# Kernel tuning notes

Measured on AMD Instinct MI355X. Metric: run time of the kernel, lower is better.

Reference implementation:

```python
import jax, jax.numpy as jnp
import numpy as np
from jax import lax

B, S, T = 128, 512, 256


def setup_inputs() -> dict:
    key = jax.random.key(0)
    k1, k2, k3, k4, k5, k6 = jax.random.split(key, 6)
    logits = jax.random.normal(k1, (B, S, T), dtype=jnp.float32)
    lengths = jax.random.randint(k2, (B,), S // 2, S + 1)
    mask = jnp.arange(S)[None, :] < lengths[:, None]  # [B,S] bool, mask[:,0] always True
    labels = jax.random.randint(k3, (B, S), 0, T)
    start_transitions = 0.1 * jax.random.normal(k4, (T,), dtype=jnp.float32)
    end_transitions = 0.1 * jax.random.normal(k5, (T,), dtype=jnp.float32)
    transitions = 0.1 * jax.random.normal(k6, (T, T), dtype=jnp.float32)
    return {"logits": logits, "mask": mask, "labels": labels,
            "start_transitions": start_transitions,
            "end_transitions": end_transitions,
            "transitions": transitions}


def _numerator(logits, tags, mask, start_t, end_t, trans):
    # Score of the gold tag path (torchcrf _compute_score), fully vectorized.
    b = jnp.arange(logits.shape[0])
    maskf = mask.astype(logits.dtype)
    emit = jnp.take_along_axis(logits, tags[..., None], axis=2)[..., 0]  # [B,S]
    score = start_t[tags[:, 0]] + emit[:, 0]
    tr = trans[tags[:, :-1], tags[:, 1:]]  # [B,S-1]
    score = score + jnp.sum((tr + emit[:, 1:]) * maskf[:, 1:], axis=1)
    lengths = mask.sum(axis=1)
    last_tags = tags[b, lengths - 1]
    return score + end_t[last_tags]


def _denominator(logits, mask, start_t, end_t, trans):
    # Forward algorithm (log partition), lax.scan over time.
    score0 = start_t[None, :] + logits[:, 0]  # [B,T]

    def step(score, xs):
        emit, m = xs  # emit [B,T], m [B]
        nxt = jax.nn.logsumexp(score[:, :, None] + trans[None, :, :]
                               + emit[:, None, :], axis=1)  # [B,T]
        return jnp.where(m[:, None], nxt, score), None

    emits = jnp.swapaxes(logits[:, 1:], 0, 1)  # [S-1,B,T]
    masks = mask[:, 1:].T  # [S-1,B]
    score, _ = lax.scan(step, score0, (emits, masks))
    return jax.nn.logsumexp(score + end_t[None, :], axis=1)  # [B]


def _viterbi(logits, mask, start_t, end_t, trans):
    # Viterbi decode with masking; masked steps carry score and use identity
    # backpointers so backtracing passes through padding correctly.
    Bn, Sn, Tn = logits.shape
    score0 = start_t[None, :] + logits[:, 0]  # [B,T]
    ident = jnp.arange(Tn, dtype=jnp.int32)[None, :]

    def step(score, xs):
        emit, m = xs
        cand = score[:, :, None] + trans[None, :, :]  # [B,T_prev,T_next]
        idx = jnp.argmax(cand, axis=1).astype(jnp.int32)  # [B,T]
        nxt = jnp.max(cand, axis=1) + emit
        score = jnp.where(m[:, None], nxt, score)
        hist = jnp.where(m[:, None], idx, ident)
        return score, hist

    emits = jnp.swapaxes(logits[:, 1:], 0, 1)
    masks = mask[:, 1:].T
    score, history = lax.scan(step, score0, (emits, masks))  # history [S-1,B,T]
    last = jnp.argmax(score + end_t[None, :], axis=1).astype(jnp.int32)  # [B]

    def back(tag, h):
        prev = jnp.take_along_axis(h, tag[:, None], axis=1)[:, 0]
        return prev, prev

    _, tags_prefix = lax.scan(back, last, history, reverse=True)  # [S-1,B]
    tags = jnp.concatenate([tags_prefix.T, last[:, None]], axis=1)  # [B,S]
    return jnp.where(mask, tags, 0)


def reference(logits, mask, labels, start_transitions, end_transitions, transitions):
    pred = _viterbi(logits, mask, start_transitions, end_transitions, transitions)
    num = _numerator(logits, labels, mask, start_transitions, end_transitions, transitions)
    den = _denominator(logits, mask, start_transitions, end_transitions, transitions)
    loss = -jnp.mean(num - den)  # torchcrf reduction='mean', negated
    return pred, loss
```

## Files before the change

kernel.cpp:

```cpp
#include <hip/hip_runtime.h>
#include <hip/hip_bf16.h>
#include <math.h>

#define Bn 128
#define Sn 512
#define Tn 256

typedef float vf64 __attribute__((ext_vector_type(64)));


__global__ void prep_kernel(const float* __restrict__ trans, float* __restrict__ transT) {
    int k = blockIdx.x * blockDim.x + threadIdx.x;
    transT[(k & 255) * 256 + (k >> 8)] = trans[k];
}

__launch_bounds__(512, 2)
__global__ void crf_fwd2_kernel(const float* __restrict__ logits,
                                const float* __restrict__ start_t,
                                const float* __restrict__ end_t,
                                const float* __restrict__ trans,
                                const void* __restrict__ mask,
                                const int* __restrict__ labels,
                                int* __restrict__ lengths_out,
                                float* __restrict__ hist,
                                float* __restrict__ den_out,
                                int* __restrict__ last_out,
                                float* __restrict__ num_out) {
    const int bid = blockIdx.x;
    const bool is_vit = bid < Bn;
    const int b = is_vit ? bid : bid - Bn;
    const int tid = threadIdx.x;
    const int jp = tid & 127;
    const int q  = tid >> 7;
    const int j0 = jp * 2, j1 = j0 + 1;
    const int i0 = q * 64;
    const int wv = tid >> 6, lane = tid & 63;

    __shared__ __align__(16) float sbuf[Tn];
    __shared__ float part[1024];
    __shared__ float msh[2];
    __shared__ int   lenred[8];
    __shared__ float wredf[8];
    __shared__ int   wredi[8];
    __shared__ float wnum[8];

    int nz;
    {
        const unsigned int* mu = (const unsigned int*)mask;
        unsigned int w0 = mu[0];
        if (w0 == 1u)                nz = (((const int*)mask)[b * Sn + tid] != 0);
        else if (w0 == 0x3F800000u)  nz = (((const float*)mask)[b * Sn + tid] != 0.0f);
        else                         nz = (((const unsigned char*)mask)[b * Sn + tid] != 0);
    }
    unsigned long long bal = __ballot(nz != 0);
    if (lane == 0) lenred[wv] = __popcll(bal);
    __syncthreads();
    int len = 0;
    #pragma unroll
    for (int w = 0; w < 8; ++w) len += lenred[w];
    if (is_vit && tid == 0) lengths_out[b] = len;

    vf64 tA, tB;
    {
        const float2* t2 = (const float2*)trans;
        if (is_vit) {
            #pragma unroll
            for (int i = 0; i < 64; ++i) {
                float2 v = t2[(size_t)(i0 + i) * 128 + jp];
                tA[i] = v.x; tB[i] = v.y;
            }
        } else {
            #pragma unroll
            for (int i = 0; i < 64; ++i) {
                float2 v = t2[(size_t)(i0 + i) * 128 + jp];
                tA[i] = __expf(v.x); tB[i] = __expf(v.y);
            }
        }
    }

    const float* lg = logits + (size_t)b * Sn * Tn + tid;
    const float4* sb4 = (const float4*)sbuf;
    const int q16 = q * 16;

    float cur = 0.0f, emit_cur = 0.0f, emit_next = 0.0f, base = 0.0f;

    if (is_vit) {
        if (tid < Tn) {
            cur = start_t[tid] + lg[0];
            sbuf[tid] = cur;
            emit_cur = lg[Tn];
        }
        __syncthreads();

        for (int t = 1; t < len; ++t) {
            if (tid < Tn) {
                int tn = (t + 1 < len) ? (t + 1) : (len - 1);
                emit_next = lg[(size_t)tn * Tn];
            }
            float b0 = -INFINITY, b1 = -INFINITY, b2 = -INFINITY, b3 = -INFINITY;
            #pragma unroll
            for (int k = 0; k < 16; ++k) {
                float4 s4 = sb4[q16 + k];
                int i = 4 * k;
                float c0 = s4.x + tA[i],     c1 = s4.y + tA[i + 1];
                float c2 = s4.z + tA[i + 2], c3 = s4.w + tA[i + 3];
                b0 = fmaxf(fmaxf(b0, c0), c1);
                b1 = fmaxf(fmaxf(b1, c2), c3);
                float d0 = s4.x + tB[i],     d1 = s4.y + tB[i + 1];
                float d2 = s4.z + tB[i + 2], d3 = s4.w + tB[i + 3];
                b2 = fmaxf(fmaxf(b2, d0), d1);
                b3 = fmaxf(fmaxf(b3, d2), d3);
            }
            part[q * 256 + j0] = fmaxf(b0, b1);
            part[q * 256 + j1] = fmaxf(b2, b3);
            __syncthreads();
            if (tid < Tn) {
                float bb = fmaxf(fmaxf(part[tid], part[256 + tid]),
                                 fmaxf(part[512 + tid], part[768 + tid]));
                hist[((size_t)t * Bn + b) * Tn + tid] = bb;
                cur = bb + emit_cur;
                emit_cur = emit_next;
                sbuf[tid] = cur;
            }
            __syncthreads();
        }

        float bv = -INFINITY; int bj = 0;
        if (tid < Tn) { bv = cur + end_t[tid]; bj = tid; }
        #pragma unroll
        for (int off = 32; off; off >>= 1) {
            float ov = __shfl_xor(bv, off);
            int   oj = __shfl_xor(bj, off);
            if (ov > bv || (ov == bv && oj < bj)) { bv = ov; bj = oj; }
        }
        if (lane == 0) { wredf[wv] = bv; wredi[wv] = bj; }
        __syncthreads();
        if (tid == 0) {
            float BB = wredf[0]; int AA = wredi[0];
            #pragma unroll
            for (int w = 1; w < 4; ++w)
                if (wredf[w] > BB || (wredf[w] == BB && wredi[w] < AA)) { BB = wredf[w]; AA = wredi[w]; }
            last_out[b] = AA;
        }
    } else {
        if (tid < Tn) {
            cur = start_t[tid] + lg[0];
            if (tid == 0) msh[0] = cur;
            emit_cur = lg[Tn];
        }
        __syncthreads();
        if (tid < Tn) {
            base = msh[0];
            sbuf[tid] = __expf(cur - base);
        }
        __syncthreads();

        for (int t = 1; t < len; ++t) {
            if (tid < Tn) {
                int tn = (t + 1 < len) ? (t + 1) : (len - 1);
                emit_next = lg[(size_t)tn * Tn];
            }
            float a0 = 0.f, a1 = 0.f, c0 = 0.f, c1 = 0.f;
            #pragma unroll
            for (int k = 0; k < 16; ++k) {
                float4 p4 = sb4[q16 + k];
                int i = 4 * k;
                a0 = fmaf(p4.x, tA[i],     a0); a1 = fmaf(p4.y, tA[i + 1], a1);
                a0 = fmaf(p4.z, tA[i + 2], a0); a1 = fmaf(p4.w, tA[i + 3], a1);
                c0 = fmaf(p4.x, tB[i],     c0); c1 = fmaf(p4.y, tB[i + 1], c1);
                c0 = fmaf(p4.z, tB[i + 2], c0); c1 = fmaf(p4.w, tB[i + 3], c1);
            }
            part[q * 256 + j0] = a0 + a1;
            part[q * 256 + j1] = c0 + c1;
            __syncthreads();
            if (tid < Tn) {
                float tot = (part[tid] + part[256 + tid]) + (part[512 + tid] + part[768 + tid]);
                float nb = msh[(t - 1) & 1];
                cur = base + __logf(tot) + emit_cur;
                emit_cur = emit_next;
                sbuf[tid] = __expf(cur - nb);
                base = nb;
                if (tid == 0) msh[t & 1] = cur;
            }
            __syncthreads();
        }

        float v2 = (tid < Tn) ? (cur + end_t[tid]) : -INFINITY;
        float wm = v2;
        #pragma unroll
        for (int off = 32; off; off >>= 1) wm = fmaxf(wm, __shfl_xor(wm, off));
        if (lane == 0) wredf[wv] = wm;
        __syncthreads();
        float M = fmaxf(fmaxf(wredf[0], wredf[1]), fmaxf(wredf[2], wredf[3]));
        float ex = (tid < Tn) ? __expf(v2 - M) : 0.0f;
        #pragma unroll
        for (int off = 32; off; off >>= 1) ex += __shfl_xor(ex, off);
        if (lane == 0) wnum[wv] = ex;
        __syncthreads();
        if (tid == 0) den_out[b] = M + __logf(wnum[0] + wnum[1] + wnum[2] + wnum[3]);
        __syncthreads();

        float acc = 0.0f;
        if (tid >= 1 && tid < len) {
            int prev = labels[b * Sn + tid - 1], curl = labels[b * Sn + tid];
            acc = trans[prev * Tn + curl] + logits[((size_t)b * Sn + tid) * Tn + curl];
        }
        #pragma unroll
        for (int off = 32; off; off >>= 1) acc += __shfl_xor(acc, off);
        if (lane == 0) wnum[wv] = acc;
        __syncthreads();
        if (tid == 0) {
            float s = 0.0f;
            #pragma unroll
            for (int w = 0; w < 8; ++w) s += wnum[w];
            int l0 = labels[b * Sn];
            int ll = labels[b * Sn + len - 1];
            num_out[b] = start_t[l0] + logits[(size_t)b * Sn * Tn + l0] + s + end_t[ll];
        }
    }
}

__global__ void bt_loss_kernel(const float* __restrict__ hist,
                               const float* __restrict__ logits,
                               const float* __restrict__ start_t,
                               const float* __restrict__ transT,
                               const int* __restrict__ last,
                               const int* __restrict__ lengths,
                               const float* __restrict__ num,
                               const float* __restrict__ den,
                               float* __restrict__ pred,
                               float* __restrict__ out_loss) {
    const int lane = threadIdx.x;
    if (blockIdx.x == Bn) {
        float v = (den[lane] - num[lane]) + (den[lane + 64] - num[lane + 64]);
        #pragma unroll
        for (int off = 32; off; off >>= 1) v += __shfl_xor(v, off);
        if (lane == 0) out_loss[0] = v * (1.0f / 128.0f);
        return;
    }
    const int b = blockIdx.x;
    const int len = lengths[b], len1 = len - 1;
    __shared__ int tg[Sn];
    int tag = last[b];
    if (lane == 0) tg[len1] = tag;
    float target = hist[((size_t)len1 * Bn + b) * Tn + tag];

    const float4* lgrow = (const float4*)(logits + (size_t)b * Sn * Tn) + lane;
    float4 s4 = *((const float4*)start_t + lane);

    float4 hbuf[4], ebuf[4];
    #pragma unroll
    for (int qq = 0; qq < 4; ++qq) {
        int r = len1 - 1 - qq;
        if (r >= 0) {
            int rh = (r > 1) ? r : 1;
            ebuf[qq] = lgrow[(size_t)r * 64];
            hbuf[qq] = *((const float4*)(hist + ((size_t)rh * Bn + b) * Tn) + lane);
        }
    }

    for (int k = 0; k < len1; ++k) {
        int r = len1 - 1 - k;
        float4 h4 = hbuf[k & 3], e4 = ebuf[k & 3];
        float4 sv;
        if (r > 0) {
            sv.x = h4.x + e4.x; sv.y = h4.y + e4.y; sv.z = h4.z + e4.z; sv.w = h4.w + e4.w;
        } else {
            sv.x = s4.x + e4.x; sv.y = s4.y + e4.y; sv.z = s4.z + e4.z; sv.w = s4.w + e4.w;
        }
        int rp = r - 4;
        if (rp >= 0) {
            int rh = (rp > 1) ? rp : 1;
            ebuf[k & 3] = lgrow[(size_t)rp * 64];
            hbuf[k & 3] = *((const float4*)(hist + ((size_t)rh * Bn + b) * Tn) + lane);
        }
        float4 t4 = *((const float4*)(transT + (size_t)tag * Tn) + lane);
        int m4 = ((sv.x + t4.x) == target ? 1 : 0)
               | ((sv.y + t4.y) == target ? 2 : 0)
               | ((sv.z + t4.z) == target ? 4 : 0)
               | ((sv.w + t4.w) == target ? 8 : 0);
        unsigned long long bb = __ballot(m4 != 0);
        int L = __ffsll(bb) - 1;
        int mm = __shfl(m4, L);
        int slot = __ffs(mm) - 1;
        tag = L * 4 + slot;
        if (lane == 0) tg[r] = tag;
        float hv = (slot == 0) ? h4.x : (slot == 1) ? h4.y : (slot == 2) ? h4.z : h4.w;
        target = __shfl(hv, L);
    }
    __syncthreads();
    for (int t = lane; t < Sn; t += 64)
        pred[(size_t)b * Sn + t] = (t < len) ? (float)tg[t] : 0.0f;
}


__global__ void compute_E_kernel(const float* __restrict__ trans, __hip_bfloat16* __restrict__ E) {
    int k = blockIdx.x * blockDim.x + threadIdx.x;
    if (k < Tn * Tn) E[k] = __float2bfloat16(__expf(trans[k]));
}

__global__ void lengths_kernel(const void* __restrict__ mask, int* __restrict__ lengths) {
    int b = blockIdx.x, tid = threadIdx.x;
    const unsigned int* mu = (const unsigned int*)mask;
    unsigned int w0 = mu[0];
    int cnt = 0;
    if (w0 == 1u) {
        const int* mi = (const int*)mask;
        for (int t = tid; t < Sn; t += 256) cnt += (mi[b * Sn + t] != 0);
    } else if (w0 == 0x3F800000u) {
        const float* mf = (const float*)mask;
        for (int t = tid; t < Sn; t += 256) cnt += (mf[b * Sn + t] != 0.0f);
    } else {
        const unsigned char* mb = (const unsigned char*)mask;
        for (int t = tid; t < Sn; t += 256) cnt += (mb[b * Sn + t] != 0);
    }
    for (int off = 32; off; off >>= 1) cnt += __shfl_xor(cnt, off);
    __shared__ int red[4];
    if ((tid & 63) == 0) red[tid >> 6] = cnt;
    __syncthreads();
    if (tid == 0) lengths[b] = red[0] + red[1] + red[2] + red[3];
}

__global__ void numerator_kernel(const float* __restrict__ logits, const int* __restrict__ labels,
                                 const float* __restrict__ start_t, const float* __restrict__ end_t,
                                 const float* __restrict__ trans, const int* __restrict__ lengths,
                                 float* __restrict__ num) {
    int b = blockIdx.x, tid = threadIdx.x;
    int len = lengths[b];
    float acc = 0.0f;
    for (int t = tid + 1; t < len; t += 256) {
        int prev = labels[b * Sn + t - 1], cur = labels[b * Sn + t];
        acc += trans[prev * Tn + cur] + logits[((size_t)b * Sn + t) * Tn + cur];
    }
    for (int off = 32; off; off >>= 1) acc += __shfl_xor(acc, off);
    __shared__ float red[4];
    if ((tid & 63) == 0) red[tid >> 6] = acc;
    __syncthreads();
    if (tid == 0) {
        int l0 = labels[b * Sn];
        int ll = labels[b * Sn + len - 1];
        num[b] = start_t[l0] + logits[(size_t)b * Sn * Tn + l0]
               + red[0] + red[1] + red[2] + red[3] + end_t[ll];
    }
}

__launch_bounds__(1024)
__global__ void fused_fwd_kernel(const float* __restrict__ logits,
                                 const float* __restrict__ start_t,
                                 const float* __restrict__ end_t,
                                 const float* __restrict__ trans,
                                 const __hip_bfloat16* __restrict__ E,
                                 const int* __restrict__ lengths,
                                 unsigned char* __restrict__ hist,
                                 float* __restrict__ den_out,
                                 int* __restrict__ last_out) {
    int b = blockIdx.x;
    int tid = threadIdx.x;
    int j = tid & 255;
    int h = tid >> 8;
    int i0 = h * 64;

    __shared__ __align__(16) float sden[Tn];
    __shared__ __align__(16) float svit[Tn];
    __shared__ __align__(16) float p[Tn];
    __shared__ float redf[16];
    __shared__ float reds[16];
    __shared__ float redb[16];
    __shared__ int   redbi[16];
    __shared__ float pd[1024];
    __shared__ float pv[1024];
    __shared__ int   pa[1024];

    int len = lengths[b];
    if (tid < Tn) {
        float v = start_t[j] + logits[(size_t)b * Sn * Tn + j];
        sden[j] = v;
        svit[j] = v;
    }
    __syncthreads();

    for (int t = 1; t < len; ++t) {
        float v = sden[j];
        for (int off = 32; off; off >>= 1) v = fmaxf(v, __shfl_xor(v, off));
        if ((tid & 63) == 0) redf[tid >> 6] = v;
        __syncthreads();
        float m = redf[0];
        #pragma unroll
        for (int w = 1; w < 16; ++w) m = fmaxf(m, redf[w]);
        if (tid < Tn) p[j] = __expf(sden[j] - m);
        __syncthreads();

        float s = 0.0f, best = -INFINITY;
        int arg = 0;
        const float* tr = trans + (size_t)i0 * Tn + j;
        const __hip_bfloat16* er = E + (size_t)i0 * Tn + j;
        #pragma unroll 4
        for (int i = i0; i < i0 + 64; i += 4) {
            float4 p4  = *(const float4*)(p + i);
            float4 sv4 = *(const float4*)(svit + i);
            float tr0 = tr[0 * Tn], tr1 = tr[1 * Tn], tr2 = tr[2 * Tn], tr3 = tr[3 * Tn];
            float e0 = __bfloat162float(er[0 * Tn]);
            float e1 = __bfloat162float(er[1 * Tn]);
            float e2 = __bfloat162float(er[2 * Tn]);
            float e3 = __bfloat162float(er[3 * Tn]);
            tr += 4 * Tn; er += 4 * Tn;
            s = fmaf(p4.x, e0, s); s = fmaf(p4.y, e1, s);
            s = fmaf(p4.z, e2, s); s = fmaf(p4.w, e3, s);
            float c0 = sv4.x + tr0; if (c0 > best) { best = c0; arg = i + 0; }
            float c1 = sv4.y + tr1; if (c1 > best) { best = c1; arg = i + 1; }
            float c2 = sv4.z + tr2; if (c2 > best) { best = c2; arg = i + 2; }
            float c3 = sv4.w + tr3; if (c3 > best) { best = c3; arg = i + 3; }
        }
        pd[tid] = s; pv[tid] = best; pa[tid] = arg;
        __syncthreads();

        if (tid < Tn) {
            float ss = pd[j] + pd[j + 256] + pd[j + 512] + pd[j + 768];
            float bb = pv[j]; int aa = pa[j];
            if (pv[j + 256] > bb) { bb = pv[j + 256]; aa = pa[j + 256]; }
            if (pv[j + 512] > bb) { bb = pv[j + 512]; aa = pa[j + 512]; }
            if (pv[j + 768] > bb) { bb = pv[j + 768]; aa = pa[j + 768]; }
            float emit = logits[((size_t)b * Sn + t) * Tn + j];
            sden[j] = m + __logf(ss) + emit;
            svit[j] = bb + emit;
            hist[((size_t)t * Bn + b) * Tn + j] = (unsigned char)aa;
        }
        __syncthreads();
    }

    float v2d = sden[j] + end_t[j];
    float M = v2d;
    for (int off = 32; off; off >>= 1) M = fmaxf(M, __shfl_xor(M, off));
    if ((tid & 63) == 0) redf[tid >> 6] = M;
    __syncthreads();
    M = redf[0];
    #pragma unroll
    for (int w = 1; w < 16; ++w) M = fmaxf(M, redf[w]);

    float ex = (tid < Tn) ? __expf(v2d - M) : 0.0f;
    for (int off = 32; off; off >>= 1) ex += __shfl_xor(ex, off);

    float v2v = svit[j] + end_t[j];
    float bv = v2v; int bj = j;
    for (int off = 32; off; off >>= 1) {
        float ov = __shfl_xor(bv, off); int oj = __shfl_xor(bj, off);
        if (ov > bv || (ov == bv && oj < bj)) { bv = ov; bj = oj; }
    }
    if ((tid & 63) == 0) { reds[tid >> 6] = ex; redb[tid >> 6] = bv; redbi[tid >> 6] = bj; }
    __syncthreads();
    if (tid == 0) {
        float sum = 0.0f;
        #pragma unroll
        for (int w = 0; w < 16; ++w) sum += reds[w];
        den_out[b] = M + __logf(sum);
        float BB = redb[0]; int AA = redbi[0];
        #pragma unroll
        for (int w = 1; w < 16; ++w)
            if (redb[w] > BB || (redb[w] == BB && redbi[w] < AA)) { BB = redb[w]; AA = redbi[w]; }
        last_out[b] = AA;
    }
}

__global__ void backtrack_kernel(const unsigned char* __restrict__ hist,
                                 const int* __restrict__ last,
                                 const int* __restrict__ lengths,
                                 float* __restrict__ pred) {
    int b = blockIdx.x, lane = threadIdx.x;
    int len = lengths[b];
    int len1 = len - 1;
    __shared__ int tg[Sn];
    int tag = last[b];

    const int P = 16;
    unsigned int buf[P];
    #pragma unroll
    for (int qq = 0; qq < P; ++qq) {
        int r = len1 - qq;
        if (qq < len1)
            buf[qq] = *(const unsigned int*)(hist + ((size_t)r * Bn + b) * Tn + lane * 4);
    }
    if (lane == 0) tg[len1] = tag;
    for (int qq = 0; qq < len1; ++qq) {
        unsigned int w = buf[qq & (P - 1)];
        int sel = __shfl((int)w, tag >> 2, 64);
        tag = (sel >> ((tag & 3) * 8)) & 255;
        int t = len1 - 1 - qq;
        if (lane == 0) tg[t] = tag;
        int rn = len1 - qq - P;
        if (rn >= 1)
            buf[qq & (P - 1)] = *(const unsigned int*)(hist + ((size_t)rn * Bn + b) * Tn + lane * 4);
    }
    __syncthreads();
    for (int t = lane; t < Sn; t += 64)
        pred[(size_t)b * Sn + t] = (t < len) ? (float)tg[t] : 0.0f;
}

__global__ void loss_kernel(const float* __restrict__ num, const float* __restrict__ den,
                            float* __restrict__ out_loss) {
    int tid = threadIdx.x;
    float v = den[tid] - num[tid];
    for (int off = 32; off; off >>= 1) v += __shfl_xor(v, off);
    __shared__ float r2[2];
    if ((tid & 63) == 0) r2[tid >> 6] = v;
    __syncthreads();
    if (tid == 0) out_loss[0] = (r2[0] + r2[1]) * (1.0f / 128.0f);
}


extern "C" void kernel_launch(void* const* d_in, const int* in_sizes, int n_in,
                              void* d_out, int out_size, void* d_ws, size_t ws_size,
                              hipStream_t stream) {
    const float* logits  = (const float*)d_in[0];
    const void*  mask    = d_in[1];
    const int*   labels  = (const int*)d_in[2];
    const float* start_t = (const float*)d_in[3];
    const float* end_t   = (const float*)d_in[4];
    const float* trans   = (const float*)d_in[5];
    float* out = (float*)d_out;

    char* ws = (char*)d_ws;
    const size_t histF = (size_t)Sn * Bn * Tn * 4;
    const size_t tblF  = (size_t)Tn * Tn * 4;
    const size_t needF = histF + tblF + 8192;

    if (ws_size >= needF) {
        float* hist    = (float*)ws;
        float* transT  = (float*)(ws + histF);
        char*  tail    = ws + histF + tblF;
        int*   lengths = (int*)tail;
        float* num     = (float*)(tail + 2048);
        float* den     = (float*)(tail + 4096);
        int*   lastp   = (int*)(tail + 6144);

        prep_kernel<<<Tn * Tn / 256, 256, 0, stream>>>(trans, transT);
        crf_fwd2_kernel<<<2 * Bn, 512, 0, stream>>>(logits, start_t, end_t, trans, mask,
                                                    labels, lengths, hist, den, lastp, num);
        bt_loss_kernel<<<Bn + 1, 64, 0, stream>>>(hist, logits, start_t, transT, lastp,
                                                  lengths, num, den, out, out + (size_t)Bn * Sn);
    } else {
        const size_t histSz = (size_t)Sn * Bn * Tn;
        unsigned char*  hist    = (unsigned char*)ws;
        int*            lengths = (int*)(ws + histSz);
        float*          num     = (float*)(ws + histSz + 512);
        float*          den     = (float*)(ws + histSz + 1024);
        int*            lastp   = (int*)(ws + histSz + 1536);
        __hip_bfloat16* E       = (__hip_bfloat16*)(ws + histSz + 2048);

        compute_E_kernel<<<(Tn * Tn) / 256, 256, 0, stream>>>(trans, E);
        lengths_kernel<<<Bn, 256, 0, stream>>>(mask, lengths);
        fused_fwd_kernel<<<Bn, 1024, 0, stream>>>(logits, start_t, end_t, trans, E,
                                                  lengths, hist, den, lastp);
        numerator_kernel<<<Bn, 256, 0, stream>>>(logits, labels, start_t, end_t, trans,
                                                 lengths, num);
        backtrack_kernel<<<Bn, 64, 0, stream>>>(hist, lastp, lengths, out);
        loss_kernel<<<1, 128, 0, stream>>>(num, den, out + (size_t)Bn * Sn);
    }
}
```

Baseline: 796.5 us.

## Use fp16 dot2 for forward recursion, repartition work over 8 row groups

The forward (log-partition) blocks now store exp(transitions) packed as fp16 pairs and do the per-step matrix-vector product with fdot2 instructions. The state probabilities are also kept in fp16, with a fixed shift to avoid underflow. Both forward and Viterbi blocks split the reduction over 8 row groups of 32, each thread producing 4 output columns instead of 2, and the cross-group reduction grows from 4 to 8 partials. The backtrace prefetch depth goes from 4 to 8 and the transT load is issued earlier. This trades fp16 precision in the loss for fewer ALU ops and registers per step, at the cost of more shared-memory reduction traffic per step.

```diff
diff --git a/kernel.cpp b/kernel.cpp
--- a/kernel.cpp
+++ b/kernel.cpp
@@ -6,19 +6,36 @@
 #define Sn 512
 #define Tn 256
 
-typedef float vf64 __attribute__((ext_vector_type(64)));
-
-
-__global__ void prep_kernel(const float* __restrict__ trans, float* __restrict__ transT) {
+typedef float vf32t __attribute__((ext_vector_type(32)));
+typedef unsigned int vu16t __attribute__((ext_vector_type(16)));
+typedef _Float16 half2_t __attribute__((ext_vector_type(2)));
+
+static __device__ inline float dot2h(unsigned int p, unsigned int e, float acc) {
+#if __has_builtin(__builtin_amdgcn_fdot2)
+    return __builtin_amdgcn_fdot2(__builtin_bit_cast(half2_t, p),
+                                  __builtin_bit_cast(half2_t, e), acc, false);
+#else
+    half2_t ph = __builtin_bit_cast(half2_t, p), eh = __builtin_bit_cast(half2_t, e);
+    return acc + (float)ph.x * (float)eh.x + (float)ph.y * (float)eh.y;
+#endif
+}
+
+
+__global__ void prep_kernel(const float* __restrict__ trans, float* __restrict__ transT,
+                            _Float16* __restrict__ E16) {
     int k = blockIdx.x * blockDim.x + threadIdx.x;
-    transT[(k & 255) * 256 + (k >> 8)] = trans[k];
+    int i = k >> 8, c = k & 255;
+    float v = trans[k];
+    transT[c * 256 + i] = v;
+    E16[((size_t)(i >> 1) * 512) + c * 2 + (i & 1)] = (_Float16)__expf(v);
 }
 
 __launch_bounds__(512, 2)
-__global__ void crf_fwd2_kernel(const float* __restrict__ logits,
+__global__ void crf_fwd3_kernel(const float* __restrict__ logits,
                                 const float* __restrict__ start_t,
                                 const float* __restrict__ end_t,
                                 const float* __restrict__ trans,
+                                const unsigned int* __restrict__ E16w,
                                 const void* __restrict__ mask,
                                 const int* __restrict__ labels,
                                 int* __restrict__ lengths_out,
@@ -30,14 +47,15 @@
     const bool is_vit = bid < Bn;
     const int b = is_vit ? bid : bid - Bn;
     const int tid = threadIdx.x;
-    const int jp = tid & 127;
-    const int q  = tid >> 7;
-    const int j0 = jp * 2, j1 = j0 + 1;
-    const int i0 = q * 64;
+    const int jp = tid & 63;
+    const int q  = tid >> 6;
+    const int j0 = jp * 4;
+    const int i0 = q * 32;
     const int wv = tid >> 6, lane = tid & 63;
 
     __shared__ __align__(16) float sbuf[Tn];
-    __shared__ float part[1024];
+    __shared__ __align__(16) _Float16 p16[Tn];
+    __shared__ __align__(16) float part[8 * Tn];
     __shared__ float msh[2];
     __shared__ int   lenred[8];
     __shared__ float wredf[8];
@@ -60,31 +78,20 @@
     for (int w = 0; w < 8; ++w) len += lenred[w];
     if (is_vit && tid == 0) lengths_out[b] = len;
 
-    vf64 tA, tB;
-    {
-        const float2* t2 = (const float2*)trans;
-        if (is_vit) {
-            #pragma unroll
-            for (int i = 0; i < 64; ++i) {
-                float2 v = t2[(size_t)(i0 + i) * 128 + jp];
-                tA[i] = v.x; tB[i] = v.y;
-            }
-        } else {
-            #pragma unroll
-            for (int i = 0; i < 64; ++i) {
-                float2 v = t2[(size_t)(i0 + i) * 128 + jp];
-                tA[i] = __expf(v.x); tB[i] = __expf(v.y);
-            }
-        }
-    }
-
     const float* lg = logits + (size_t)b * Sn * Tn + tid;
     const float4* sb4 = (const float4*)sbuf;
-    const int q16 = q * 16;
-
-    float cur = 0.0f, emit_cur = 0.0f, emit_next = 0.0f, base = 0.0f;
+    const unsigned int* p16w = (const unsigned int*)p16;
+
+    float cur = 0.0f, emit_cur = 0.0f, emit_next = 0.0f;
 
     if (is_vit) {
+        vf32t tvA, tvB, tvC, tvD;
+        #pragma unroll
+        for (int r = 0; r < 32; ++r) {
+            float4 v = *(const float4*)(trans + (size_t)(i0 + r) * Tn + j0);
+            tvA[r] = v.x; tvB[r] = v.y; tvC[r] = v.z; tvD[r] = v.w;
+        }
+
         if (tid < Tn) {
             cur = start_t[tid] + lg[0];
             sbuf[tid] = cur;
@@ -97,26 +104,30 @@
                 int tn = (t + 1 < len) ? (t + 1) : (len - 1);
                 emit_next = lg[(size_t)tn * Tn];
             }
-            float b0 = -INFINITY, b1 = -INFINITY, b2 = -INFINITY, b3 = -INFINITY;
+            float bA = -INFINITY, bB = -INFINITY, bC = -INFINITY, bD = -INFINITY;
             #pragma unroll
-            for (int k = 0; k < 16; ++k) {
-                float4 s4 = sb4[q16 + k];
+            for (int k = 0; k < 8; ++k) {
+                float4 s4 = sb4[q * 8 + k];
                 int i = 4 * k;
-                float c0 = s4.x + tA[i],     c1 = s4.y + tA[i + 1];
-                float c2 = s4.z + tA[i + 2], c3 = s4.w + tA[i + 3];
-                b0 = fmaxf(fmaxf(b0, c0), c1);
-                b1 = fmaxf(fmaxf(b1, c2), c3);
-                float d0 = s4.x + tB[i],     d1 = s4.y + tB[i + 1];
-                float d2 = s4.z + tB[i + 2], d3 = s4.w + tB[i + 3];
-                b2 = fmaxf(fmaxf(b2, d0), d1);
-                b3 = fmaxf(fmaxf(b3, d2), d3);
+                float cA0 = s4.x + tvA[i],     cA1 = s4.y + tvA[i + 1];
+                float cA2 = s4.z + tvA[i + 2], cA3 = s4.w + tvA[i + 3];
+                bA = fmaxf(fmaxf(bA, cA0), cA1); bA = fmaxf(fmaxf(bA, cA2), cA3);
+                float cB0 = s4.x + tvB[i],     cB1 = s4.y + tvB[i + 1];
+                float cB2 = s4.z + tvB[i + 2], cB3 = s4.w + tvB[i + 3];
+                bB = fmaxf(fmaxf(bB, cB0), cB1); bB = fmaxf(fmaxf(bB, cB2), cB3);
+                float cC0 = s4.x + tvC[i],     cC1 = s4.y + tvC[i + 1];
+                float cC2 = s4.z + tvC[i + 2], cC3 = s4.w + tvC[i + 3];
+                bC = fmaxf(fmaxf(bC, cC0), cC1); bC = fmaxf(fmaxf(bC, cC2), cC3);
+                float cD0 = s4.x + tvD[i],     cD1 = s4.y + tvD[i + 1];
+                float cD2 = s4.z + tvD[i + 2], cD3 = s4.w + tvD[i + 3];
+                bD = fmaxf(fmaxf(bD, cD0), cD1); bD = fmaxf(fmaxf(bD, cD2), cD3);
             }
-            part[q * 256 + j0] = fmaxf(b0, b1);
-            part[q * 256 + j1] = fmaxf(b2, b3);
+            *(float4*)(part + q * Tn + j0) = make_float4(bA, bB, bC, bD);
             __syncthreads();
             if (tid < Tn) {
-                float bb = fmaxf(fmaxf(part[tid], part[256 + tid]),
-                                 fmaxf(part[512 + tid], part[768 + tid]));
+                float bb = part[tid];
+                #pragma unroll
+                for (int q2 = 1; q2 < 8; ++q2) bb = fmaxf(bb, part[q2 * Tn + tid]);
                 hist[((size_t)t * Bn + b) * Tn + tid] = bb;
                 cur = bb + emit_cur;
                 emit_cur = emit_next;
@@ -143,6 +154,15 @@
             last_out[b] = AA;
         }
     } else {
+        vu16t tdA, tdB, tdC, tdD;
+        #pragma unroll
+        for (int k = 0; k < 16; ++k) {
+            uint4 v = *(const uint4*)(E16w + (size_t)(16 * q + k) * Tn + j0);
+            tdA[k] = v.x; tdB[k] = v.y; tdC[k] = v.z; tdD[k] = v.w;
+        }
+
+        const float SHIFT = 9.0f;
+        float pbase = 0.0f;
         if (tid < Tn) {
             cur = start_t[tid] + lg[0];
             if (tid == 0) msh[0] = cur;
@@ -150,8 +170,8 @@
         }
         __syncthreads();
         if (tid < Tn) {
-            base = msh[0];
-            sbuf[tid] = __expf(cur - base);
+            pbase = msh[0] + SHIFT;
+            p16[tid] = (_Float16)__expf(cur - pbase);
         }
         __syncthreads();
 
@@ -160,26 +180,27 @@
                 int tn = (t + 1 < len) ? (t + 1) : (len - 1);
                 emit_next = lg[(size_t)tn * Tn];
             }
-            float a0 = 0.f, a1 = 0.f, c0 = 0.f, c1 = 0.f;
+            float sA = 0.f, sB = 0.f, sC = 0.f, sD = 0.f;
             #pragma unroll
-            for (int k = 0; k < 16; ++k) {
-                float4 p4 = sb4[q16 + k];
-                int i = 4 * k;
-                a0 = fmaf(p4.x, tA[i],     a0); a1 = fmaf(p4.y, tA[i + 1], a1);
-                a0 = fmaf(p4.z, tA[i + 2], a0); a1 = fmaf(p4.w, tA[i + 3], a1);
-                c0 = fmaf(p4.x, tB[i],     c0); c1 = fmaf(p4.y, tB[i + 1], c1);
-                c0 = fmaf(p4.z, tB[i + 2], c0); c1 = fmaf(p4.w, tB[i + 3], c1);
+            for (int k = 0; k < 8; ++k) {
+                uint2 pp = *(const uint2*)(p16w + q * 16 + 2 * k);
+                int i = 2 * k;
+                sA = dot2h(pp.x, tdA[i], sA); sA = dot2h(pp.y, tdA[i + 1], sA);
+                sB = dot2h(pp.x, tdB[i], sB); sB = dot2h(pp.y, tdB[i + 1], sB);
+                sC = dot2h(pp.x, tdC[i], sC); sC = dot2h(pp.y, tdC[i + 1], sC);
+                sD = dot2h(pp.x, tdD[i], sD); sD = dot2h(pp.y, tdD[i + 1], sD);
             }
-            part[q * 256 + j0] = a0 + a1;
-            part[q * 256 + j1] = c0 + c1;
+            *(float4*)(part + q * Tn + j0) = make_float4(sA, sB, sC, sD);
             __syncthreads();
             if (tid < Tn) {
-                float tot = (part[tid] + part[256 + tid]) + (part[512 + tid] + part[768 + tid]);
+                float tot = part[tid];
+                #pragma unroll
+                for (int q2 = 1; q2 < 8; ++q2) tot += part[q2 * Tn + tid];
                 float nb = msh[(t - 1) & 1];
-                cur = base + __logf(tot) + emit_cur;
+                cur = pbase + __logf(tot) + emit_cur;
                 emit_cur = emit_next;
-                sbuf[tid] = __expf(cur - nb);
-                base = nb;
+                p16[tid] = (_Float16)__expf(cur - nb - SHIFT);
+                pbase = nb + SHIFT;
                 if (tid == 0) msh[t & 1] = cur;
             }
             __syncthreads();
@@ -246,35 +267,37 @@
     float target = hist[((size_t)len1 * Bn + b) * Tn + tag];
 
     const float4* lgrow = (const float4*)(logits + (size_t)b * Sn * Tn) + lane;
+    const char* histb = (const char*)(hist + (size_t)b * Tn);
     float4 s4 = *((const float4*)start_t + lane);
 
-    float4 hbuf[4], ebuf[4];
+    const int PF = 8;
+    float4 hbuf[PF], ebuf[PF];
     #pragma unroll
-    for (int qq = 0; qq < 4; ++qq) {
+    for (int qq = 0; qq < PF; ++qq) {
         int r = len1 - 1 - qq;
         if (r >= 0) {
             int rh = (r > 1) ? r : 1;
             ebuf[qq] = lgrow[(size_t)r * 64];
-            hbuf[qq] = *((const float4*)(hist + ((size_t)rh * Bn + b) * Tn) + lane);
+            hbuf[qq] = *((const float4*)(histb + (size_t)rh * (Bn * Tn * 4)) + lane);
         }
     }
 
     for (int k = 0; k < len1; ++k) {
         int r = len1 - 1 - k;
-        float4 h4 = hbuf[k & 3], e4 = ebuf[k & 3];
+        float4 t4 = *((const float4*)(transT + (size_t)tag * Tn) + lane);
+        float4 h4 = hbuf[k & (PF - 1)], e4 = ebuf[k & (PF - 1)];
+        int rp = r - PF;
+        if (rp >= 0) {
+            int rh = (rp > 1) ? rp : 1;
+            ebuf[k & (PF - 1)] = lgrow[(size_t)rp * 64];
+            hbuf[k & (PF - 1)] = *((const float4*)(histb + (size_t)rh * (Bn * Tn * 4)) + lane);
+        }
         float4 sv;
         if (r > 0) {
             sv.x = h4.x + e4.x; sv.y = h4.y + e4.y; sv.z = h4.z + e4.z; sv.w = h4.w + e4.w;
         } else {
             sv.x = s4.x + e4.x; sv.y = s4.y + e4.y; sv.z = s4.z + e4.z; sv.w = s4.w + e4.w;
         }
-        int rp = r - 4;
-        if (rp >= 0) {
-            int rh = (rp > 1) ? rp : 1;
-            ebuf[k & 3] = lgrow[(size_t)rp * 64];
-            hbuf[k & 3] = *((const float4*)(hist + ((size_t)rh * Bn + b) * Tn) + lane);
-        }
-        float4 t4 = *((const float4*)(transT + (size_t)tag * Tn) + lane);
         int m4 = ((sv.x + t4.x) == target ? 1 : 0)
                | ((sv.y + t4.y) == target ? 2 : 0)
                | ((sv.z + t4.z) == target ? 4 : 0)
@@ -521,19 +544,22 @@
     char* ws = (char*)d_ws;
     const size_t histF = (size_t)Sn * Bn * Tn * 4;
     const size_t tblF  = (size_t)Tn * Tn * 4;
-    const size_t needF = histF + tblF + 8192;
+    const size_t e16F  = (size_t)Tn * Tn * 2;
+    const size_t needF = histF + tblF + e16F + 8192;
 
     if (ws_size >= needF) {
-        float* hist    = (float*)ws;
-        float* transT  = (float*)(ws + histF);
-        char*  tail    = ws + histF + tblF;
-        int*   lengths = (int*)tail;
-        float* num     = (float*)(tail + 2048);
-        float* den     = (float*)(tail + 4096);
-        int*   lastp   = (int*)(tail + 6144);
-
-        prep_kernel<<<Tn * Tn / 256, 256, 0, stream>>>(trans, transT);
-        crf_fwd2_kernel<<<2 * Bn, 512, 0, stream>>>(logits, start_t, end_t, trans, mask,
+        float*        hist    = (float*)ws;
+        float*        transT  = (float*)(ws + histF);
+        _Float16*     E16     = (_Float16*)(ws + histF + tblF);
+        char*         tail    = ws + histF + tblF + e16F;
+        int*          lengths = (int*)tail;
+        float*        num     = (float*)(tail + 2048);
+        float*        den     = (float*)(tail + 4096);
+        int*          lastp   = (int*)(tail + 6144);
+
+        prep_kernel<<<Tn * Tn / 256, 256, 0, stream>>>(trans, transT, E16);
+        crf_fwd3_kernel<<<2 * Bn, 512, 0, stream>>>(logits, start_t, end_t, trans,
+                                                    (const unsigned int*)E16, mask,
                                                     labels, lengths, hist, den, lastp, num);
         bt_loss_kernel<<<Bn + 1, 64, 0, stream>>>(hist, logits, start_t, transT, lastp,
                                                   lengths, num, den, out, out + (size_t)Bn * Sn);
```

Measured after the change: 792.7 us. No clear change (-0.5%).
